# Performance work log

Hardware: AMD Instinct MI355X
Metric: run time of the kernel (lower is better)

The kernel has to match this reference:

```python
import jax, jax.numpy as jnp
import numpy as np

B, S, D, H, DFF, C, E = 8, 1024, 1024, 16, 4096, 16, 8
HD = D // H


def setup_inputs() -> dict:
    key = jax.random.key(0)
    ks = jax.random.split(key, 24)
    g = lambda k, shape, fan: jax.random.normal(k, shape, jnp.float32) * (fan ** -0.5)
    inp = {
        'x': jax.random.normal(ks[0], (B, S, D), jnp.float32),
        # attention params
        'Wqkv': g(ks[1], (D, 3 * D), D), 'bqkv': jnp.zeros((3 * D,), jnp.float32),
        'Wo': g(ks[2], (D, D), D), 'bo': jnp.zeros((D,), jnp.float32),
        'ln1_g': jnp.ones((D,), jnp.float32), 'ln1_b': jnp.zeros((D,), jnp.float32),
        # base FFN params
        'W1': g(ks[3], (D, DFF), D), 'b1': jnp.zeros((DFF,), jnp.float32),
        'W2': g(ks[4], (DFF, D), DFF), 'b2': jnp.zeros((D,), jnp.float32),
        # longtail expert FFN stacks [E, ...] (original zero-inits second linear; random here for a meaningful baseline)
        'eW1': g(ks[5], (E, D, DFF), D), 'eb1': jnp.zeros((E, DFF), jnp.float32),
        'eW2': g(ks[6], (E, DFF, D), DFF), 'eb2': jnp.zeros((E, D), jnp.float32),
        'ln2_g': jnp.ones((D,), jnp.float32), 'ln2_b': jnp.zeros((D,), jnp.float32),
        # routing centers/radii; first E centers are longtail
        'centers': jax.random.normal(ks[7], (C, D), jnp.float32),
        'radius': jax.random.uniform(ks[8], (C,), jnp.float32, 0.5, 1.5),
        'center_to_expert': jnp.concatenate([jnp.arange(E, dtype=jnp.int32), -jnp.ones((C - E,), jnp.int32)]),
    }
    return inp


def _ln(x, gamma, beta, eps=1e-5):
    mu = x.mean(-1, keepdims=True)
    var = ((x - mu) ** 2).mean(-1, keepdims=True)
    return (x - mu) * jax.lax.rsqrt(var + eps) * gamma + beta


def _mha(x, Wqkv, bqkv, Wo, bo):
    b, s, d = x.shape
    qkv = x @ Wqkv + bqkv  # [b,s,3d]
    q, k, v = jnp.split(qkv, 3, axis=-1)
    q = q.reshape(b, s, H, HD).transpose(0, 2, 1, 3)
    k = k.reshape(b, s, H, HD).transpose(0, 2, 1, 3)
    v = v.reshape(b, s, H, HD).transpose(0, 2, 1, 3)
    scores = jnp.einsum('bhqd,bhkd->bhqk', q, k) / np.sqrt(HD).astype(np.float32)
    attn = jax.nn.softmax(scores, axis=-1)
    out = jnp.einsum('bhqk,bhkd->bhqd', attn, v)
    out = out.transpose(0, 2, 1, 3).reshape(b, s, d)
    return out @ Wo + bo


def reference(x, Wqkv, bqkv, Wo, bo, ln1_g, ln1_b, W1, b1, W2, b2,
              eW1, eb1, eW2, eb2, ln2_g, ln2_b, centers, radius, center_to_expert):
    # get_attn_output: post-LN residual attention
    h = _ln(x + _mha(x, Wqkv, bqkv, Wo, bo), ln1_g, ln1_b)  # [B,S,D]
    # base FFN output (without LN)
    base_ffn = jax.nn.gelu(h @ W1 + b1) @ W2 + b2  # [B,S,D]
    # cal_ffn_indices: per-sample routing on mean-pooled (detached) features
    pooled = jax.lax.stop_gradient(h.mean(1))  # [B,D]
    dists = jnp.linalg.norm(pooled[:, None, :] - centers[None, :, :], axis=-1) / radius  # [B,C]
    labels = jnp.argmin(dists, axis=1)  # [B]
    eidx = center_to_expert[labels]  # [B], -1 if not longtail
    mask = (eidx >= 0)
    eidx_c = jnp.maximum(eidx, 0)
    # per-sample expert FFN (grouped gather instead of python loop)
    hmid = jax.nn.gelu(jnp.einsum('bsd,bdf->bsf', h, eW1[eidx_c]) + eb1[eidx_c][:, None, :])
    expert_out = jnp.einsum('bsf,bfd->bsd', hmid, eW2[eidx_c]) + eb2[eidx_c][:, None, :]
    ffn_out = base_ffn + jnp.where(mask[:, None, None], expert_out, 0.0)
    out = _ln(h + ffn_out, ln2_g, ln2_b)
    return out, labels
```

## Files before the change

kernel.cpp:

```cpp
#include <hip/hip_runtime.h>

#define BB 8
#define SS 1024
#define DD 1024
#define HH 16
#define HDIM 64
#define DFFV 4096

typedef __bf16 bf16x8 __attribute__((ext_vector_type(8)));
typedef float f32x4 __attribute__((ext_vector_type(4)));

__device__ __forceinline__ unsigned short f2bf(float f){
  unsigned int u = __float_as_uint(f);
  u += 0x7fffu + ((u >> 16) & 1u);
  return (unsigned short)(u >> 16);
}
__device__ __forceinline__ float bf2f(unsigned short s){
  return __uint_as_float(((unsigned int)s) << 16);
}
__device__ __forceinline__ float ldf(const void* p, long i, bool isbf){
  return isbf ? bf2f(((const unsigned short*)p)[i]) : ((const float*)p)[i];
}
__device__ __forceinline__ float gelu_f(float x){
  float x3 = x*x*x;
  return 0.5f*x*(1.f + tanhf(0.7978845608028654f*(x + 0.044715f*x3)));
}

__global__ void detect_kernel(const unsigned int* __restrict__ g, int* __restrict__ flag){
  *flag = (g[0] == 0x3F803F80u) ? 1 : 0;
}

__global__ __launch_bounds__(256)
void convert_x_kernel(const void* __restrict__ src, unsigned short* __restrict__ dst,
                      const int* __restrict__ flag){
  bool isbf = *flag != 0;
  long i = (long)blockIdx.x*256 + threadIdx.x;
  if (isbf){
    ((uint4*)dst)[i] = ((const uint4*)src)[i];
  } else {
    const float4* s = (const float4*)src + i*2;
    float4 a = s[0], b = s[1];
    uint4 o;
    o.x = (unsigned)f2bf(a.x) | ((unsigned)f2bf(a.y)<<16);
    o.y = (unsigned)f2bf(a.z) | ((unsigned)f2bf(a.w)<<16);
    o.z = (unsigned)f2bf(b.x) | ((unsigned)f2bf(b.y)<<16);
    o.w = (unsigned)f2bf(b.z) | ((unsigned)f2bf(b.w)<<16);
    ((uint4*)dst)[i] = o;
  }
}

__global__ __launch_bounds__(256)
void transpose_w_kernel(const void* __restrict__ src, unsigned short* __restrict__ dst,
                        int K, int N, const int* __restrict__ usedflags,
                        long srcBatch, long dstBatch, const int* __restrict__ flag){
  if (usedflags && usedflags[blockIdx.z] == 0) return;
  bool isbf = *flag != 0;
  long soff = (long)blockIdx.z * srcBatch;
  dst += (long)blockIdx.z * dstBatch;
  __shared__ float tile[64][65];
  int t = threadIdx.x;
  int r = t >> 2, c0 = (t & 3) * 16;
  int kt = blockIdx.y * 64, nt = blockIdx.x * 64;
  long base = soff + (long)(kt + r) * N + nt + c0;
  float vals[16];
  if (isbf){
    const unsigned short* s = (const unsigned short*)src + base;
    uint4 u0 = *(const uint4*)s, u1 = *(const uint4*)(s + 8);
    unsigned int w[8] = {u0.x,u0.y,u0.z,u0.w,u1.x,u1.y,u1.z,u1.w};
    #pragma unroll
    for (int k=0;k<8;k++){ vals[2*k] = __uint_as_float(w[k]<<16); vals[2*k+1] = __uint_as_float(w[k]&0xFFFF0000u); }
  } else {
    const float4* s = (const float4*)((const float*)src + base);
    #pragma unroll
    for (int k=0;k<4;k++){ float4 v = s[k]; vals[4*k]=v.x; vals[4*k+1]=v.y; vals[4*k+2]=v.z; vals[4*k+3]=v.w; }
  }
  #pragma unroll
  for (int j=0;j<16;j++) tile[r][c0+j] = vals[j];
  __syncthreads();
  float ov[16];
  #pragma unroll
  for (int j=0;j<16;j++) ov[j] = tile[c0+j][r];
  unsigned int p[8];
  #pragma unroll
  for (int j=0;j<8;j++) p[j] = (unsigned)f2bf(ov[2*j]) | ((unsigned)f2bf(ov[2*j+1])<<16);
  uint4 o0, o1;
  o0.x=p[0]; o0.y=p[1]; o0.z=p[2]; o0.w=p[3];
  o1.x=p[4]; o1.y=p[5]; o1.z=p[6]; o1.w=p[7];
  uint4* d = (uint4*)(dst + (long)(nt + r)*K + kt + c0);
  d[0]=o0; d[1]=o1;
}

template<int EPI>
__global__ __launch_bounds__(256, 2)
void gemm_bt(const unsigned short* __restrict__ A, const unsigned short* __restrict__ Bt,
             void* __restrict__ Cv, const void* __restrict__ bias,
             const void* __restrict__ resid, int M, int N, int K,
             const int* __restrict__ eidx, long Ab, long Bb, long Cb, long biasb,
             const int* __restrict__ flag)
{
  int z = blockIdx.z;
  long boff = 0;
  if (eidx){
    int e = eidx[z];
    if (e < 0) return;
    Bt += (long)e * Bb;
    boff = (long)e * biasb;
  }
  A += (long)z * Ab;
  long coff = (long)z * Cb;

  __shared__ __align__(16) unsigned short Al[128][40];
  __shared__ __align__(16) unsigned short Bl[128][40];

  int t = threadIdx.x;
  int wave = t >> 6, lane = t & 63;
  int wm = (wave >> 1) * 64, wn = (wave & 1) * 64;
  int lr = lane & 15, lk = (lane >> 4) * 8;
  int tm = blockIdx.y * 128, tn = blockIdx.x * 128;

  int sr = t >> 2, sc = (t & 3) * 8;
  const uint4* ga0 = (const uint4*)(A + (long)(tm + sr) * K + sc);
  const uint4* ga1 = (const uint4*)(A + (long)(tm + sr + 64) * K + sc);
  const uint4* gb0 = (const uint4*)(Bt + (long)(tn + sr) * K + sc);
  const uint4* gb1 = (const uint4*)(Bt + (long)(tn + sr + 64) * K + sc);

  f32x4 acc[4][4] = {};

  int niter = K >> 5;
  for (int it = 0; it < niter; ++it){
    uint4 va0 = *ga0, va1 = *ga1, vb0 = *gb0, vb1 = *gb1;
    ga0 += 4; ga1 += 4; gb0 += 4; gb1 += 4;
    __syncthreads();
    *(uint4*)&Al[sr][sc]    = va0;
    *(uint4*)&Al[sr+64][sc] = va1;
    *(uint4*)&Bl[sr][sc]    = vb0;
    *(uint4*)&Bl[sr+64][sc] = vb1;
    __syncthreads();
    bf16x8 af[4], bfv[4];
    #pragma unroll
    for (int i=0;i<4;i++) af[i]  = *(const bf16x8*)&Al[wm + i*16 + lr][lk];
    #pragma unroll
    for (int i=0;i<4;i++) bfv[i] = *(const bf16x8*)&Bl[wn + i*16 + lr][lk];
    #pragma unroll
    for (int mt=0;mt<4;mt++)
      #pragma unroll
      for (int nt=0;nt<4;nt++)
        acc[mt][nt] = __builtin_amdgcn_mfma_f32_16x16x32_bf16(af[mt], bfv[nt], acc[mt][nt], 0, 0, 0);
  }

  bool isbf = *flag != 0;
  #pragma unroll
  for (int mt=0; mt<4; mt++){
    int gm = tm + wm + mt*16 + (lane>>4)*4;
    #pragma unroll
    for (int nt=0; nt<4; nt++){
      int gn = tn + wn + nt*16 + lr;
      float bv = ldf(bias, boff + gn, isbf);
      #pragma unroll
      for (int r=0;r<4;r++){
        float v = acc[mt][nt][r] + bv;
        long idx = coff + (long)(gm + r) * N + gn;
        if (EPI == 0)      ((unsigned short*)Cv)[idx] = f2bf(v);
        else if (EPI == 1) ((float*)Cv)[idx] = v + ldf(resid, idx, isbf);
        else if (EPI == 2) ((unsigned short*)Cv)[idx] = f2bf(gelu_f(v));
        else if (EPI == 3) ((float*)Cv)[idx] = v;
        else               ((float*)Cv)[idx] += v;
      }
    }
  }
}

__global__ __launch_bounds__(256)
void transpose_v_kernel(const unsigned short* __restrict__ qkv, unsigned short* __restrict__ vT){
  int bh = blockIdx.y; int b = bh >> 4, h = bh & 15;
  int s0 = blockIdx.x * 64;
  __shared__ __align__(16) unsigned short tile[64][72];
  int t = threadIdx.x;
  int r = t >> 2, c = t & 3;
  const uint4* src = (const uint4*)(qkv + (long)(b*SS + s0 + r)*3072 + 2048 + h*HDIM + c*16);
  uint4 v0 = src[0], v1 = src[1];
  *(uint4*)&tile[r][c*16]   = v0;
  *(uint4*)&tile[r][c*16+8] = v1;
  __syncthreads();
  int hd = t >> 2; int sc = (t & 3) * 16;
  unsigned int p[8];
  #pragma unroll
  for (int j=0;j<8;j++){
    unsigned short a  = tile[sc + 2*j][hd];
    unsigned short b2 = tile[sc + 2*j + 1][hd];
    p[j] = (unsigned)a | ((unsigned)b2 << 16);
  }
  uint4 o0, o1;
  o0.x=p[0];o0.y=p[1];o0.z=p[2];o0.w=p[3];
  o1.x=p[4];o1.y=p[5];o1.z=p[6];o1.w=p[7];
  uint4* d = (uint4*)(vT + ((long)(b*HH + h)*HDIM + hd)*SS + s0 + sc);
  d[0]=o0; d[1]=o1;
}

__global__ __launch_bounds__(256, 2)
void flash_kernel(const unsigned short* __restrict__ qkv, const unsigned short* __restrict__ vT,
                  unsigned short* __restrict__ attn)
{
  int bh = blockIdx.y; int b = bh >> 4, h = bh & 15;
  int q0 = blockIdx.x * 64;
  int t = threadIdx.x, wave = t >> 6, lane = t & 63;
  int lr = lane & 15, lq = lane >> 4, lk = lq * 8;

  __shared__ __align__(16) unsigned short Kl[64][72];
  __shared__ __align__(16) unsigned short Vl[64][72];
  __shared__ __align__(16) unsigned short Pl[4][16][72];

  bf16x8 qf[2];
  {
    const unsigned short* qrow = qkv + (long)(b*SS + q0 + wave*16 + lr)*3072 + h*HDIM;
    #pragma unroll
    for (int kt=0;kt<2;kt++){
      uint4 u = *(const uint4*)(qrow + kt*32 + lk);
      qf[kt] = __builtin_bit_cast(bf16x8, u);
    }
  }

  f32x4 O[4] = {};
  float mrow[4] = {-1e30f,-1e30f,-1e30f,-1e30f};
  float lrow[4] = {0.f,0.f,0.f,0.f};

  int sr = t >> 2, scn = (t & 3) * 16;
  const unsigned short* kbase = qkv + (long)(b*SS)*3072 + 1024 + h*HDIM;
  const unsigned short* vbase = vT + ((long)(b*HH + h)*HDIM + sr)*SS;

  for (int kb = 0; kb < SS; kb += 64){
    __syncthreads();
    {
      const uint4* sk = (const uint4*)(kbase + (long)(kb + sr)*3072 + scn);
      uint4 k0 = sk[0], k1 = sk[1];
      const uint4* sv = (const uint4*)(vbase + kb + scn);
      uint4 w0 = sv[0], w1 = sv[1];
      *(uint4*)&Kl[sr][scn]   = k0;
      *(uint4*)&Kl[sr][scn+8] = k1;
      *(uint4*)&Vl[sr][scn]   = w0;
      *(uint4*)&Vl[sr][scn+8] = w1;
    }
    __syncthreads();

    f32x4 sf[4];
    #pragma unroll
    for (int nt=0;nt<4;nt++){
      f32x4 a = {};
      #pragma unroll
      for (int kt=0;kt<2;kt++){
        bf16x8 kf = *(const bf16x8*)&Kl[nt*16 + lr][kt*32 + lk];
        a = __builtin_amdgcn_mfma_f32_16x16x32_bf16(qf[kt], kf, a, 0, 0, 0);
      }
      sf[nt] = a * 0.125f;
    }
    #pragma unroll
    for (int r=0;r<4;r++){
      float m0 = fmaxf(fmaxf(sf[0][r], sf[1][r]), fmaxf(sf[2][r], sf[3][r]));
      m0 = fmaxf(m0, __shfl_xor(m0, 1));
      m0 = fmaxf(m0, __shfl_xor(m0, 2));
      m0 = fmaxf(m0, __shfl_xor(m0, 4));
      m0 = fmaxf(m0, __shfl_xor(m0, 8));
      float mn = fmaxf(mrow[r], m0);
      float alpha = __expf(mrow[r] - mn);
      mrow[r] = mn;
      float rs = 0.f;
      float pv[4];
      #pragma unroll
      for (int nt=0;nt<4;nt++){
        float p = __expf(sf[nt][r] - mn);
        pv[nt] = p; rs += p;
      }
      rs += __shfl_xor(rs, 1); rs += __shfl_xor(rs, 2);
      rs += __shfl_xor(rs, 4); rs += __shfl_xor(rs, 8);
      lrow[r] = lrow[r]*alpha + rs;
      #pragma unroll
      for (int nt=0;nt<4;nt++) O[nt][r] *= alpha;
      int prow = lq*4 + r;
      #pragma unroll
      for (int nt=0;nt<4;nt++) Pl[wave][prow][nt*16 + lr] = f2bf(pv[nt]);
    }
    __syncthreads();
    bf16x8 pf[2];
    #pragma unroll
    for (int kt=0;kt<2;kt++) pf[kt] = *(const bf16x8*)&Pl[wave][lr][kt*32 + lk];
    #pragma unroll
    for (int nt=0;nt<4;nt++){
      #pragma unroll
      for (int kt=0;kt<2;kt++){
        bf16x8 vf = *(const bf16x8*)&Vl[nt*16 + lr][kt*32 + lk];
        O[nt] = __builtin_amdgcn_mfma_f32_16x16x32_bf16(pf[kt], vf, O[nt], 0, 0, 0);
      }
    }
  }
  #pragma unroll
  for (int r=0;r<4;r++){
    float inv = 1.f / lrow[r];
    int q = q0 + wave*16 + lq*4 + r;
    #pragma unroll
    for (int nt=0;nt<4;nt++){
      attn[(long)(b*SS + q)*DD + h*HDIM + nt*16 + lr] = f2bf(O[nt][r] * inv);
    }
  }
}

__global__ __launch_bounds__(256)
void ln_kernel(const float* __restrict__ xin, const float* __restrict__ addin,
               const void* __restrict__ gamma, const void* __restrict__ beta,
               void* __restrict__ outp, int outDual, unsigned short* __restrict__ outbf,
               const int* __restrict__ flag)
{
  bool isbf = *flag != 0;
  int row = blockIdx.x, t = threadIdx.x;
  __shared__ float red[8];
  float4 v = ((const float4*)(xin + (long)row*DD))[t];
  if (addin){
    float4 a = ((const float4*)(addin + (long)row*DD))[t];
    v.x += a.x; v.y += a.y; v.z += a.z; v.w += a.w;
  }
  float s = v.x + v.y + v.z + v.w;
  #pragma unroll
  for (int o=32;o>0;o>>=1) s += __shfl_down(s, o);
  if ((t & 63) == 0) red[t>>6] = s;
  __syncthreads();
  if (t == 0) red[4] = red[0]+red[1]+red[2]+red[3];
  __syncthreads();
  float mean = red[4] * (1.f/1024.f);
  float dx = v.x-mean, dy = v.y-mean, dz = v.z-mean, dw = v.w-mean;
  float s2 = dx*dx + dy*dy + dz*dz + dw*dw;
  __syncthreads();
  #pragma unroll
  for (int o=32;o>0;o>>=1) s2 += __shfl_down(s2, o);
  if ((t & 63) == 0) red[t>>6] = s2;
  __syncthreads();
  if (t == 0) red[4] = red[0]+red[1]+red[2]+red[3];
  __syncthreads();
  float rstd = rsqrtf(red[4] * (1.f/1024.f) + 1e-5f);
  int c = t*4;
  float o0 = dx*rstd*ldf(gamma,c+0,isbf) + ldf(beta,c+0,isbf);
  float o1 = dy*rstd*ldf(gamma,c+1,isbf) + ldf(beta,c+1,isbf);
  float o2 = dz*rstd*ldf(gamma,c+2,isbf) + ldf(beta,c+2,isbf);
  float o3 = dw*rstd*ldf(gamma,c+3,isbf) + ldf(beta,c+3,isbf);
  if (outp){
    if (outDual && isbf){
      uint2 pk;
      pk.x = (unsigned)f2bf(o0) | ((unsigned)f2bf(o1)<<16);
      pk.y = (unsigned)f2bf(o2) | ((unsigned)f2bf(o3)<<16);
      *(uint2*)((unsigned short*)outp + (long)row*DD + c) = pk;
    } else {
      float4 ov; ov.x=o0; ov.y=o1; ov.z=o2; ov.w=o3;
      ((float4*)((float*)outp + (long)row*DD))[t] = ov;
    }
  }
  if (outbf){
    uint2 pk;
    pk.x = (unsigned)f2bf(o0) | ((unsigned)f2bf(o1)<<16);
    pk.y = (unsigned)f2bf(o2) | ((unsigned)f2bf(o3)<<16);
    *(uint2*)(outbf + (long)row*DD + c) = pk;
  }
}

__global__ __launch_bounds__(256)
void pool_kernel(const float* __restrict__ h, float* __restrict__ pooled){
  int b = blockIdx.z;
  int d = blockIdx.x*256 + threadIdx.x;
  int s0 = blockIdx.y * 128;
  const float* p = h + ((long)(b*SS + s0))*DD + d;
  float s = 0.f;
  #pragma unroll 4
  for (int i=0;i<128;i++) s += p[(long)i*DD];
  atomicAdd(&pooled[b*DD + d], s * (1.f/1024.f));
}

__global__ __launch_bounds__(512)
void route_kernel(const float* __restrict__ pooled, const void* __restrict__ centers,
                  const void* __restrict__ radius, const int* __restrict__ c2e,
                  void* __restrict__ dout, int* __restrict__ eidx, int* __restrict__ usedf,
                  const int* __restrict__ flag)
{
  bool isbf = *flag != 0;
  int t = threadIdx.x;
  __shared__ float dist[8][16];
  if (t < 8) usedf[t] = 0;
  int w = t >> 6, lane = t & 63;
  int c = lane >> 2, part = lane & 3;
  const float* pb = pooled + w*1024;
  float s = 0.f;
  for (int i=0;i<256;i++){
    int d = part + i*4;
    float df = pb[d] - ldf(centers, (long)c*1024 + d, isbf);
    s += df*df;
  }
  s += __shfl_xor(s, 1);
  s += __shfl_xor(s, 2);
  if (part == 0) dist[w][c] = sqrtf(s) / ldf(radius, c, isbf);
  __syncthreads();
  if (t < 8){
    int best = 0; float bd = dist[t][0];
    #pragma unroll
    for (int cc=1;cc<16;cc++){ float dv = dist[t][cc]; if (dv < bd){ bd=dv; best=cc; } }
    if (isbf) ((unsigned short*)dout)[8388608 + t] = f2bf((float)best);
    else      ((float*)dout)[8388608 + t] = (float)best;
    int e = c2e[best];
    eidx[t] = e;
    if (e >= 0) atomicExch(&usedf[e], 1);
  }
}

extern "C" void kernel_launch(void* const* d_in, const int* in_sizes, int n_in,
                              void* d_out, int out_size, void* d_ws, size_t ws_size,
                              hipStream_t stream)
{
  (void)in_sizes; (void)n_in; (void)out_size; (void)ws_size;
  const void* x      = d_in[0];
  const void* Wqkv   = d_in[1];
  const void* bqkv   = d_in[2];
  const void* Wo     = d_in[3];
  const void* bo     = d_in[4];
  const void* ln1g   = d_in[5];
  const void* ln1b   = d_in[6];
  const void* W1     = d_in[7];
  const void* b1     = d_in[8];
  const void* W2     = d_in[9];
  const void* b2     = d_in[10];
  const void* eW1    = d_in[11];
  const void* eb1    = d_in[12];
  const void* eW2    = d_in[13];
  const void* eb2    = d_in[14];
  const void* ln2g   = d_in[15];
  const void* ln2b   = d_in[16];
  const void* centers= d_in[17];
  const void* radius = d_in[18];
  const int*  c2e    = (const int*)d_in[19];

  char* ws = (char*)d_ws;
  unsigned short* Wqkv_t = (unsigned short*)(ws + 0);
  unsigned short* Wo_t   = (unsigned short*)(ws + 6291456);
  unsigned short* W1_t   = (unsigned short*)(ws + 8388608);
  unsigned short* W2_t   = (unsigned short*)(ws + 16777216);
  float*  hbuf   = (float*)(ws + 25165824);
  unsigned short* h_bf   = (unsigned short*)(ws + 58720256);
  float*  pooled = (float*)(ws + 75497472);
  int*    eidx   = (int*)(ws + 75530240);
  int*    usedf  = (int*)(ws + 75530272);
  int*    flag   = (int*)(ws + 75530304);
  char* RA = ws + 83886080;
  unsigned short* x_bf    = (unsigned short*)(RA);
  unsigned short* vT      = (unsigned short*)(RA + 16777216);
  unsigned short* qkv_bf  = (unsigned short*)(RA + 33554432);
  unsigned short* attn_bf = (unsigned short*)(RA + 83886080);
  float*  ybuf = (float*)(RA);
  unsigned short* eWt = (unsigned short*)(RA);
  unsigned short* mid = (unsigned short*)(ws + 184549376);
  float*  ffn = (float*)(ws + 251658240);

  dim3 blk(256);

  detect_kernel<<<dim3(1), dim3(1), 0, stream>>>((const unsigned int*)ln1g, flag);
  convert_x_kernel<<<dim3(4096), blk, 0, stream>>>(x, x_bf, flag);
  transpose_w_kernel<<<dim3(48, 16), blk, 0, stream>>>(Wqkv, Wqkv_t, 1024, 3072, nullptr, 0, 0, flag);
  transpose_w_kernel<<<dim3(16, 16), blk, 0, stream>>>(Wo,   Wo_t,   1024, 1024, nullptr, 0, 0, flag);
  transpose_w_kernel<<<dim3(64, 16), blk, 0, stream>>>(W1,   W1_t,   1024, 4096, nullptr, 0, 0, flag);
  transpose_w_kernel<<<dim3(16, 64), blk, 0, stream>>>(W2,   W2_t,   4096, 1024, nullptr, 0, 0, flag);
  gemm_bt<0><<<dim3(24, 64), blk, 0, stream>>>(x_bf, Wqkv_t, qkv_bf, bqkv, nullptr,
                                               8192, 3072, 1024, nullptr, 0,0,0,0, flag);
  transpose_v_kernel<<<dim3(16, 128), blk, 0, stream>>>(qkv_bf, vT);
  flash_kernel<<<dim3(16, 128), blk, 0, stream>>>(qkv_bf, vT, attn_bf);
  gemm_bt<1><<<dim3(8, 64), blk, 0, stream>>>(attn_bf, Wo_t, ybuf, bo, x,
                                              8192, 1024, 1024, nullptr, 0,0,0,0, flag);
  ln_kernel<<<dim3(8192), blk, 0, stream>>>(ybuf, nullptr, ln1g, ln1b, hbuf, 0, h_bf, flag);
  hipMemsetAsync(pooled, 0, 32768, stream);
  pool_kernel<<<dim3(4, 8, 8), blk, 0, stream>>>(hbuf, pooled);
  route_kernel<<<dim3(1), dim3(512), 0, stream>>>(pooled, centers, radius, c2e, d_out, eidx, usedf, flag);
  transpose_w_kernel<<<dim3(64, 16, 8), blk, 0, stream>>>(eW1, eWt, 1024, 4096, usedf, 4194304, 4194304, flag);
  gemm_bt<2><<<dim3(32, 64), blk, 0, stream>>>(h_bf, W1_t, mid, b1, nullptr,
                                               8192, 4096, 1024, nullptr, 0,0,0,0, flag);
  gemm_bt<3><<<dim3(8, 64), blk, 0, stream>>>(mid, W2_t, ffn, b2, nullptr,
                                              8192, 1024, 4096, nullptr, 0,0,0,0, flag);
  gemm_bt<2><<<dim3(32, 8, 8), blk, 0, stream>>>(h_bf, eWt, mid, eb1, nullptr,
                                                 1024, 4096, 1024, eidx, 1048576, 4194304, 4194304, 4096, flag);
  transpose_w_kernel<<<dim3(16, 64, 8), blk, 0, stream>>>(eW2, eWt, 4096, 1024, usedf, 4194304, 4194304, flag);
  gemm_bt<4><<<dim3(8, 8, 8), blk, 0, stream>>>(mid, eWt, ffn, eb2, nullptr,
                                                1024, 1024, 4096, eidx, 4194304, 4194304, 1048576, 1024, flag);
  ln_kernel<<<dim3(8192), blk, 0, stream>>>(hbuf, ffn, ln2g, ln2b, d_out, 1, nullptr, flag);
}
```

Measured before the change: 858.8 us.

## Load GEMM tiles directly from global memory into LDS

Result: no change. 851.4 us (-0.9%).

```diff
diff --git a/kernel.cpp b/kernel.cpp
--- a/kernel.cpp
+++ b/kernel.cpp
@@ -24,6 +24,13 @@
 __device__ __forceinline__ float gelu_f(float x){
   float x3 = x*x*x;
   return 0.5f*x*(1.f + tanhf(0.7978845608028654f*(x + 0.044715f*x3)));
+}
+
+__device__ __forceinline__ void gload_lds16(const void* g, void* l){
+  __builtin_amdgcn_global_load_lds(
+    (const __attribute__((address_space(1))) unsigned int*)(unsigned long long)g,
+    (__attribute__((address_space(3))) unsigned int*)(unsigned int)(unsigned long long)l,
+    16, 0, 0);
 }
 
 __global__ void detect_kernel(const unsigned int* __restrict__ g, int* __restrict__ flag){
@@ -109,8 +116,8 @@
   A += (long)z * Ab;
   long coff = (long)z * Cb;
 
-  __shared__ __align__(16) unsigned short Al[128][40];
-  __shared__ __align__(16) unsigned short Bl[128][40];
+  __shared__ __align__(16) unsigned short Al[128][32];
+  __shared__ __align__(16) unsigned short Bl[128][32];
 
   int t = threadIdx.x;
   int wave = t >> 6, lane = t & 63;
@@ -118,23 +125,26 @@
   int lr = lane & 15, lk = (lane >> 4) * 8;
   int tm = blockIdx.y * 128, tn = blockIdx.x * 128;
 
-  int sr = t >> 2, sc = (t & 3) * 8;
-  const uint4* ga0 = (const uint4*)(A + (long)(tm + sr) * K + sc);
-  const uint4* ga1 = (const uint4*)(A + (long)(tm + sr + 64) * K + sc);
-  const uint4* gb0 = (const uint4*)(Bt + (long)(tn + sr) * K + sc);
-  const uint4* gb1 = (const uint4*)(Bt + (long)(tn + sr + 64) * K + sc);
+  int srow = wave*32 + (lane >> 2);
+  int scol = (lane & 3) * 8;
+  const unsigned short* gA = A + (long)(tm + srow) * K + scol;
+  const unsigned short* gB = Bt + (long)(tn + srow) * K + scol;
+  unsigned short* lA0 = &Al[wave*32][0];
+  unsigned short* lA1 = &Al[wave*32 + 16][0];
+  unsigned short* lB0 = &Bl[wave*32][0];
+  unsigned short* lB1 = &Bl[wave*32 + 16][0];
+  long rstep = (long)16 * K;
 
   f32x4 acc[4][4] = {};
 
   int niter = K >> 5;
   for (int it = 0; it < niter; ++it){
-    uint4 va0 = *ga0, va1 = *ga1, vb0 = *gb0, vb1 = *gb1;
-    ga0 += 4; ga1 += 4; gb0 += 4; gb1 += 4;
     __syncthreads();
-    *(uint4*)&Al[sr][sc]    = va0;
-    *(uint4*)&Al[sr+64][sc] = va1;
-    *(uint4*)&Bl[sr][sc]    = vb0;
-    *(uint4*)&Bl[sr+64][sc] = vb1;
+    gload_lds16(gA,         lA0);
+    gload_lds16(gA + rstep, lA1);
+    gload_lds16(gB,         lB0);
+    gload_lds16(gB + rstep, lB1);
+    gA += 32; gB += 32;
     __syncthreads();
     bf16x8 af[4], bfv[4];
     #pragma unroll
```
